# Optimization experiments

Measured on AMD Instinct MI355X. Metric: run time of the kernel, lower is better.

The kernel has to match this reference:

```python
import jax, jax.numpy as jnp
import numpy as np

V = 100000   # vertices
C = 64       # in channels
D = 64       # out channels
W = 8        # weight matrices
DEG = 16     # neighbors per vertex
E = V * DEG  # edges


def setup_inputs() -> dict:
    key = jax.random.key(0)
    k = jax.random.split(key, 6)
    data = jax.random.normal(k[0], (V, C), dtype=jnp.float32)
    # fixed-degree adjacency: vertex i has DEG neighbors (arbitrary dst)
    edge_src = jnp.repeat(jnp.arange(V, dtype=jnp.int32), DEG)        # [E] sorted
    edge_dst = jax.random.randint(k[1], (E,), 0, V, dtype=jnp.int32)  # [E]
    edge_vals = jnp.full((E,), 1.0 / DEG, dtype=jnp.float32)          # row-normalized
    var_u = 0.1 * jax.random.normal(k[2], (C, W), dtype=jnp.float32)
    var_c = 0.1 * jax.random.normal(k[3], (W,), dtype=jnp.float32)
    var_w = 0.1 * jax.random.normal(k[4], (W, C, D), dtype=jnp.float32)
    var_b = 0.1 * jax.random.normal(k[5], (D,), dtype=jnp.float32)
    return {"data": data, "edge_src": edge_src, "edge_dst": edge_dst,
            "edge_vals": edge_vals, "var_u": var_u, "var_c": var_c,
            "var_w": var_w, "var_b": var_b}


def reference(data, edge_src, edge_dst, edge_vals, var_u, var_c, var_w, var_b):
    # translation_invariant=True => var_v = -var_u
    num_v = data.shape[0]
    x_u = data @ var_u            # [V, W]
    x_v = data @ (-var_u)         # [V, W]
    # edge logits and exp-normalize over the W weight matrices (softmax == exp/sum)
    logits = x_u[edge_src] + x_v[edge_dst] + var_c   # [E, W]
    q = jax.nn.softmax(logits, axis=-1)              # [E, W]
    # gathered neighbor features, pre-scaled by adjacency values
    x_sep = data[edge_dst] * edge_vals[:, None]      # [E, C]
    y = jnp.zeros((num_v, var_w.shape[-1]), dtype=data.dtype)
    for m in range(var_c.shape[0]):  # small fixed loop over W weight matrices
        agg = jax.ops.segment_sum(q[:, m:m + 1] * x_sep, edge_src,
                                  num_segments=num_v)  # [V, C]
        y = y + agg @ var_w[m]                          # [V, D]
    return y + var_b
```

## Files before the change

### kernel.cpp

```cpp
#include <hip/hip_runtime.h>

typedef _Float16 half2_t __attribute__((ext_vector_type(2)));
typedef _Float16 half8_t __attribute__((ext_vector_type(8)));
typedef __attribute__((ext_vector_type(4))) float f32x4;

#define NV 100000
#define NTILE 6250
#define GRID 512
#define LDSZ 81920

#define VMWAIT(N) asm volatile("s_waitcnt vmcnt(" #N ")" ::: "memory")
#define LGKM0     asm volatile("s_waitcnt lgkmcnt(0)" ::: "memory")
#define FENCE     asm volatile("" ::: "memory")

__device__ __forceinline__ unsigned cvt_pk_u(float a, float b) {
  auto h = __builtin_amdgcn_cvt_pkrtz(a, b);
  return __builtin_bit_cast(unsigned, h);
}
__device__ __forceinline__ half2_t u2h(unsigned u) { return __builtin_bit_cast(half2_t, u); }
__device__ __forceinline__ unsigned h2u(half2_t h) { return __builtin_bit_cast(unsigned, h); }
__device__ __forceinline__ unsigned dup_lo(unsigned q) {
  return __builtin_amdgcn_perm(q, q, 0x01000100u);
}
__device__ __forceinline__ unsigned dup_hi(unsigned q) {
  return __builtin_amdgcn_perm(q, q, 0x03020302u);
}
__device__ __forceinline__ void load16_to_lds(const void* g, void* s) {
  __builtin_amdgcn_global_load_lds(
      (const __attribute__((address_space(1))) unsigned int*)g,
      (__attribute__((address_space(3))) unsigned int*)s, 16, 0, 0);
}

__global__ __launch_bounds__(256) void k0_prep_w(const float* __restrict__ var_w,
                                                 unsigned short* __restrict__ Bt) {
  int t = blockIdx.x * 256 + threadIdx.x;
  if (t >= 64 * 512) return;
  int d = t >> 9, k = t & 511;
  _Float16 h = (_Float16)var_w[k * 64 + d];
  Bt[t] = __builtin_bit_cast(unsigned short, h);
}

__global__ __launch_bounds__(256) void k1_prep(const float* __restrict__ data,
                                               const float* __restrict__ var_u,
                                               unsigned short* __restrict__ data_h,
                                               unsigned short* __restrict__ xu_h) {
  __shared__ float u_lds[512];
  int tid = threadIdx.x;
  u_lds[tid] = var_u[tid];
  u_lds[tid + 256] = var_u[tid + 256];
  __syncthreads();
  int v = blockIdx.x * 256 + tid;
  if (v >= NV) return;
  const float4* dp = (const float4*)(data + v * 64);
  float acc[8];
#pragma unroll
  for (int w = 0; w < 8; ++w) acc[w] = 0.f;
  uint4* ob = (uint4*)(data_h + v * 64);
#pragma unroll
  for (int q = 0; q < 8; ++q) {
    float4 a4 = dp[q * 2], b4 = dp[q * 2 + 1];
    int c0 = q * 8;
#pragma unroll
    for (int w = 0; w < 8; ++w)
      acc[w] += a4.x * u_lds[(c0 + 0) * 8 + w] + a4.y * u_lds[(c0 + 1) * 8 + w]
              + a4.z * u_lds[(c0 + 2) * 8 + w] + a4.w * u_lds[(c0 + 3) * 8 + w]
              + b4.x * u_lds[(c0 + 4) * 8 + w] + b4.y * u_lds[(c0 + 5) * 8 + w]
              + b4.z * u_lds[(c0 + 6) * 8 + w] + b4.w * u_lds[(c0 + 7) * 8 + w];
    uint4 pk;
    pk.x = cvt_pk_u(a4.x, a4.y); pk.y = cvt_pk_u(a4.z, a4.w);
    pk.z = cvt_pk_u(b4.x, b4.y); pk.w = cvt_pk_u(b4.z, b4.w);
    ob[q] = pk;
  }
  uint4 xp;
  xp.x = cvt_pk_u(acc[0], acc[1]); xp.y = cvt_pk_u(acc[2], acc[3]);
  xp.z = cvt_pk_u(acc[4], acc[5]); xp.w = cvt_pk_u(acc[6], acc[7]);
  *(uint4*)(xu_h + v * 8) = xp;
}

__global__ __launch_bounds__(256, 2) void k2_main(
    const unsigned short* __restrict__ data_h,
    const unsigned short* __restrict__ xu_h,
    const int* __restrict__ edge_dst,
    const float* __restrict__ edge_vals,
    const unsigned short* __restrict__ Bt,
    const float* __restrict__ var_c,
    const float* __restrict__ var_b,
    float* __restrict__ y) {
  extern __shared__ __align__(16) char smem[];
  char* XB0  = smem;
  char* XUD0 = smem + 65536;
  char* LIN0 = smem + 73728;

  int tid = threadIdx.x;
  int wave = tid >> 6;
  int l = tid & 63;
  int q4 = l >> 4;
  int row = l & 15;
  int col = row + wave * 16;
  int lsw = (l & 56) | ((l & 7) ^ q4);

  uint4 btf[16];
#pragma unroll
  for (int ks = 0; ks < 16; ++ks)
    btf[ks] = *(const uint4*)(Bt + (col * 512 + ks * 32 + q4 * 8));
  float c8[8];
#pragma unroll
  for (int m = 0; m < 8; ++m) c8[m] = var_c[m];
  float bias = var_b[col];

#define LIN_DMA(SL, TS)                                                        \
  { char* lb_ = LIN0 + (SL) * 2048;                                            \
    if ((wave & 1) == 0)                                                       \
      load16_to_lds(edge_dst + (size_t)(TS) * 256 + l * 4, lb_);               \
    else                                                                       \
      load16_to_lds(edge_vals + (size_t)(TS) * 256 + l * 4, lb_ + 1024); }
#define XUD_DMA(SL, LSL)                                                       \
  { const int* ld_ = (const int*)(LIN0 + (LSL) * 2048);                        \
    int dv_ = ld_[wave * 64 + lsw];                                            \
    load16_to_lds(xu_h + (size_t)dv_ * 8, XUD0 + (SL) * 4096 + wave * 1024); }
#define X_DMA(SL, LSL)                                                         \
  { const int* ld_ = (const int*)(LIN0 + (LSL) * 2048);                        \
    _Pragma("unroll")                                                          \
    for (int s_ = 0; s_ < 8; ++s_) {                                           \
      int r_ = wave * 64 + s_ * 8 + (l >> 3);                                  \
      int dv_ = ld_[r_];                                                       \
      load16_to_lds(data_h + (size_t)dv_ * 64 + (l & 7) * 8,                   \
                    XB0 + (SL) * 32768 + (wave * 64 + s_ * 8) * 128); } }

  int t0 = blockIdx.x;
  int tG1 = (t0 + GRID < NTILE) ? t0 + GRID : t0;
  int tG2 = (t0 + 2 * GRID < NTILE) ? t0 + 2 * GRID : t0;
  FENCE;
  LIN_DMA(0, t0);
  LIN_DMA(1, tG1);
  LIN_DMA(2, tG2);
  FENCE;
  uint4 xsA = *(const uint4*)(xu_h + ((size_t)t0 * 16 + wave * 4 + q4) * 8);
  uint4 xsB = *(const uint4*)(xu_h + ((size_t)tG1 * 16 + wave * 4 + q4) * 8);
  VMWAIT(0);
  __builtin_amdgcn_s_barrier();
  FENCE;
  XUD_DMA(0, 0);
  X_DMA(0, 0);
  FENCE;
  VMWAIT(0);
  __builtin_amdgcn_s_barrier();

  int kc = 0;
  for (int t = t0; t < NTILE; t += GRID, ++kc) {
    int slc = kc & 1, lslc = kc & 3;
    int sl1 = (kc + 1) & 1, lsl1 = (kc + 1) & 3, lsl3 = (kc + 3) & 3;
    int t2c = (t + 2 * GRID < NTILE) ? t + 2 * GRID : t;
    int t3c = (t + 3 * GRID < NTILE) ? t + 3 * GRID : t;
    const char* XBt = XB0 + slc * 32768;
    char* XUDt = XUD0 + slc * 4096;
    const char* LINt = LIN0 + lslc * 2048;

    FENCE;
    XUD_DMA(sl1, lsl1);
    X_DMA(sl1, lsl1);
    FENCE;

    {
      uint4 xd4 = *(const uint4*)(XUDt + (wave * 64 + l) * 16);
      float evv = ((const float*)(LINt + 1024))[wave * 64 + lsw];
      half2_t xm01 = u2h(xsA.x), xm23 = u2h(xsA.y), xm45 = u2h(xsA.z), xm67 = u2h(xsA.w);
      half2_t xd01 = u2h(xd4.x), xd23 = u2h(xd4.y), xd45 = u2h(xd4.z), xd67 = u2h(xd4.w);
      float ex0 = __expf((float)xm01[0] - (float)xd01[0] + c8[0]);
      float ex1 = __expf((float)xm01[1] - (float)xd01[1] + c8[1]);
      float ex2 = __expf((float)xm23[0] - (float)xd23[0] + c8[2]);
      float ex3 = __expf((float)xm23[1] - (float)xd23[1] + c8[3]);
      float ex4 = __expf((float)xm45[0] - (float)xd45[0] + c8[4]);
      float ex5 = __expf((float)xm45[1] - (float)xd45[1] + c8[5]);
      float ex6 = __expf((float)xm67[0] - (float)xd67[0] + c8[6]);
      float ex7 = __expf((float)xm67[1] - (float)xd67[1] + c8[7]);
      float ssum = ((ex0 + ex1) + (ex2 + ex3)) + ((ex4 + ex5) + (ex6 + ex7));
      float rs = __builtin_amdgcn_rcpf(ssum) * evv;
      uint4 qq;
      qq.x = cvt_pk_u(ex0 * rs, ex1 * rs);
      qq.y = cvt_pk_u(ex2 * rs, ex3 * rs);
      qq.z = cvt_pk_u(ex4 * rs, ex5 * rs);
      qq.w = cvt_pk_u(ex6 * rs, ex7 * rs);
      *(uint4*)(XUDt + (wave * 64 + l) * 16) = qq;
    }

    uint4 xsC = *(const uint4*)(xu_h + ((size_t)t2c * 16 + wave * 4 + q4) * 8);
    FENCE;
    LIN_DMA(lsl3, t3c);
    FENCE;

    {
      int v = q4, ck = row;
      half2_t acc2[16];
#pragma unroll
      for (int i = 0; i < 16; ++i) acc2[i] = half2_t{(_Float16)0, (_Float16)0};
#pragma unroll
      for (int j = 0; j < 16; ++j) {
        int qslot = v * 16 + (j & 8) + ((j & 7) ^ v);
        uint4 qv = *(const uint4*)(XUDt + (wave * 64 + qslot) * 16);
        uint2 xx = *(const uint2*)(XBt + (size_t)(wave * 64 + v * 16 + j) * 128 + ck * 8);
        half2_t xlo = u2h(xx.x), xhi = u2h(xx.y);
        unsigned qu;
        qu = qv.x;
        acc2[0]  += xlo * u2h(dup_lo(qu)); acc2[1]  += xhi * u2h(dup_lo(qu));
        acc2[2]  += xlo * u2h(dup_hi(qu)); acc2[3]  += xhi * u2h(dup_hi(qu));
        qu = qv.y;
        acc2[4]  += xlo * u2h(dup_lo(qu)); acc2[5]  += xhi * u2h(dup_lo(qu));
        acc2[6]  += xlo * u2h(dup_hi(qu)); acc2[7]  += xhi * u2h(dup_hi(qu));
        qu = qv.z;
        acc2[8]  += xlo * u2h(dup_lo(qu)); acc2[9]  += xhi * u2h(dup_lo(qu));
        acc2[10] += xlo * u2h(dup_hi(qu)); acc2[11] += xhi * u2h(dup_hi(qu));
        qu = qv.w;
        acc2[12] += xlo * u2h(dup_lo(qu)); acc2[13] += xhi * u2h(dup_lo(qu));
        acc2[14] += xlo * u2h(dup_hi(qu)); acc2[15] += xhi * u2h(dup_hi(qu));
      }
      int vg = wave * 4 + v;
      char* ab = (char*)XBt + vg * 2048;
#pragma unroll
      for (int m = 0; m < 8; ++m) {
        int bo = (m * 128 + ck * 8) ^ ((vg & 7) << 4);
        uint2 w2;
        w2.x = h2u(acc2[2 * m]);
        w2.y = h2u(acc2[2 * m + 1]);
        *(uint2*)(ab + bo) = w2;
      }
    }
    LGKM0;
    __builtin_amdgcn_s_barrier();

    {
      f32x4 C = {0.f, 0.f, 0.f, 0.f};
#pragma unroll
      for (int ks = 0; ks < 16; ++ks) {
        int bo = (ks * 64 + q4 * 16) ^ ((row & 7) << 4);
        half8_t af = *(const half8_t*)(XBt + row * 2048 + bo);
        C = __builtin_amdgcn_mfma_f32_16x16x32_f16(
            af, __builtin_bit_cast(half8_t, btf[ks]), C, 0, 0, 0);
      }
#pragma unroll
      for (int i = 0; i < 4; ++i)
        y[(size_t)(t * 16 + q4 * 4 + i) * 64 + col] = C[i] + bias;
    }
    LGKM0;
    VMWAIT(4);
    __builtin_amdgcn_s_barrier();

    xsA = xsB; xsB = xsC;
  }
  VMWAIT(0);
#undef LIN_DMA
#undef XUD_DMA
#undef X_DMA
}

extern "C" void kernel_launch(void* const* d_in, const int* in_sizes, int n_in,
                              void* d_out, int out_size, void* d_ws, size_t ws_size,
                              hipStream_t stream) {
  const float* data      = (const float*)d_in[0];
  const int*   edge_dst  = (const int*)d_in[2];
  const float* edge_vals = (const float*)d_in[3];
  const float* var_u     = (const float*)d_in[4];
  const float* var_c     = (const float*)d_in[5];
  const float* var_w     = (const float*)d_in[6];
  const float* var_b     = (const float*)d_in[7];
  float* y = (float*)d_out;

  char* ws = (char*)d_ws;
  unsigned short* data_h = (unsigned short*)ws;
  unsigned short* xu_h   = (unsigned short*)(ws + 12800000);
  unsigned short* Bt     = (unsigned short*)(ws + 14400000);

  hipFuncSetAttribute((const void*)k2_main,
                      hipFuncAttributeMaxDynamicSharedMemorySize, LDSZ);

  hipLaunchKernelGGL(k0_prep_w, dim3(128), dim3(256), 0, stream, var_w, Bt);
  hipLaunchKernelGGL(k1_prep, dim3((NV + 255) / 256), dim3(256), 0, stream,
                     data, var_u, data_h, xu_h);
  hipLaunchKernelGGL(k2_main, dim3(GRID), dim3(256), LDSZ, stream,
                     data_h, xu_h, edge_dst, edge_vals, Bt, var_c, var_b, y);
}
```

Measured before the change: 82.86 us.

## Compute per-vertex q-weighted aggregation with MFMA and transposed LDS reads

Replaces the packed-half2 VALU loop that forms the per-vertex 16-neighbor by 8-weight aggregation with 16x16x16 f16 MFMAs. It uses ds_read_b64_tr_b16 to read the gathered neighbor features transposed. The LDS layouts of the gathered rows, the q softmax weights and the aggregate tile are reorganized with new swizzles to suit the MFMA operands. Accumulation now happens in fp32 instead of fp16. Half of each MFMA output is discarded because only 8 weight columns are real, and the final aggregate write is restricted to rows below 8.

```diff
diff --git a/kernel.cpp b/kernel.cpp
--- a/kernel.cpp
+++ b/kernel.cpp
@@ -1,6 +1,7 @@
 #include <hip/hip_runtime.h>
 
 typedef _Float16 half2_t __attribute__((ext_vector_type(2)));
+typedef _Float16 half4_t __attribute__((ext_vector_type(4)));
 typedef _Float16 half8_t __attribute__((ext_vector_type(8)));
 typedef __attribute__((ext_vector_type(4))) float f32x4;
 
@@ -18,12 +19,8 @@
   return __builtin_bit_cast(unsigned, h);
 }
 __device__ __forceinline__ half2_t u2h(unsigned u) { return __builtin_bit_cast(half2_t, u); }
-__device__ __forceinline__ unsigned h2u(half2_t h) { return __builtin_bit_cast(unsigned, h); }
-__device__ __forceinline__ unsigned dup_lo(unsigned q) {
-  return __builtin_amdgcn_perm(q, q, 0x01000100u);
-}
-__device__ __forceinline__ unsigned dup_hi(unsigned q) {
-  return __builtin_amdgcn_perm(q, q, 0x03020302u);
+__device__ __forceinline__ unsigned lds_off(const void* p) {
+  return (unsigned)(size_t)(const __attribute__((address_space(3))) char*)p;
 }
 __device__ __forceinline__ void load16_to_lds(const void* g, void* s) {
   __builtin_amdgcn_global_load_lds(
@@ -97,7 +94,6 @@
   int q4 = l >> 4;
   int row = l & 15;
   int col = row + wave * 16;
-  int lsw = (l & 56) | ((l & 7) ^ q4);
 
   uint4 btf[16];
 #pragma unroll
@@ -116,16 +112,18 @@
       load16_to_lds(edge_vals + (size_t)(TS) * 256 + l * 4, lb_ + 1024); }
 #define XUD_DMA(SL, LSL)                                                       \
   { const int* ld_ = (const int*)(LIN0 + (LSL) * 2048);                        \
-    int dv_ = ld_[wave * 64 + lsw];                                            \
+    int dv_ = ld_[wave * 64 + l];                                              \
     load16_to_lds(xu_h + (size_t)dv_ * 8, XUD0 + (SL) * 4096 + wave * 1024); }
 #define X_DMA(SL, LSL)                                                         \
   { const int* ld_ = (const int*)(LIN0 + (LSL) * 2048);                        \
+    int j_ = ((l >> 3) & 3) * 4 + ((l >> 1) & 3);                              \
+    int ch0_ = ((l >> 5) << 1) | (l & 1);                                      \
     _Pragma("unroll")                                                          \
     for (int s_ = 0; s_ < 8; ++s_) {                                           \
-      int r_ = wave * 64 + s_ * 8 + (l >> 3);                                  \
-      int dv_ = ld_[r_];                                                       \
-      load16_to_lds(data_h + (size_t)dv_ * 64 + (l & 7) * 8,                   \
-                    XB0 + (SL) * 32768 + (wave * 64 + s_ * 8) * 128); } }
+      int dv_ = ld_[wave * 64 + (s_ >> 1) * 16 + j_];                          \
+      int ch_ = ch0_ + (s_ & 1) * 4;                                           \
+      load16_to_lds(data_h + (size_t)dv_ * 64 + ch_ * 8,                       \
+                    XB0 + (SL) * 32768 + wave * 8192 + s_ * 1024); } }
 
   int t0 = blockIdx.x;
   int tG1 = (t0 + GRID < NTILE) ? t0 + GRID : t0;
@@ -152,7 +150,7 @@
     int sl1 = (kc + 1) & 1, lsl1 = (kc + 1) & 3, lsl3 = (kc + 3) & 3;
     int t2c = (t + 2 * GRID < NTILE) ? t + 2 * GRID : t;
     int t3c = (t + 3 * GRID < NTILE) ? t + 3 * GRID : t;
-    const char* XBt = XB0 + slc * 32768;
+    char* XBt = XB0 + slc * 32768;
     char* XUDt = XUD0 + slc * 4096;
     const char* LINt = LIN0 + lslc * 2048;
 
@@ -163,7 +161,7 @@
 
     {
       uint4 xd4 = *(const uint4*)(XUDt + (wave * 64 + l) * 16);
-      float evv = ((const float*)(LINt + 1024))[wave * 64 + lsw];
+      float evv = ((const float*)(LINt + 1024))[wave * 64 + l];
       half2_t xm01 = u2h(xsA.x), xm23 = u2h(xsA.y), xm45 = u2h(xsA.z), xm67 = u2h(xsA.w);
       half2_t xd01 = u2h(xd4.x), xd23 = u2h(xd4.y), xd45 = u2h(xd4.z), xd67 = u2h(xd4.w);
       float ex0 = __expf((float)xm01[0] - (float)xd01[0] + c8[0]);
@@ -181,7 +179,14 @@
       qq.y = cvt_pk_u(ex2 * rs, ex3 * rs);
       qq.z = cvt_pk_u(ex4 * rs, ex5 * rs);
       qq.w = cvt_pk_u(ex6 * rs, ex7 * rs);
-      *(uint4*)(XUDt + (wave * 64 + l) * 16) = qq;
+      int vv = l >> 4, jq = (l >> 2) & 3, jl = l & 3;
+      char* qb = XUDt + wave * 1024 + vv * 256;
+#pragma unroll
+      for (int m = 0; m < 8; ++m) {
+        unsigned short hv = (unsigned short)((&qq.x)[m >> 1] >> ((m & 1) * 16));
+        int byte = (((m ^ vv) & 7) << 5) + (((jq ^ vv ^ m) & 3) << 3) + jl * 2;
+        *(unsigned short*)(qb + byte) = hv;
+      }
     }
 
     uint4 xsC = *(const uint4*)(xu_h + ((size_t)t2c * 16 + wave * 4 + q4) * 8);
@@ -190,39 +195,51 @@
     FENCE;
 
     {
-      int v = q4, ck = row;
-      half2_t acc2[16];
-#pragma unroll
-      for (int i = 0; i < 16; ++i) acc2[i] = half2_t{(_Float16)0, (_Float16)0};
-#pragma unroll
-      for (int j = 0; j < 16; ++j) {
-        int qslot = v * 16 + (j & 8) + ((j & 7) ^ v);
-        uint4 qv = *(const uint4*)(XUDt + (wave * 64 + qslot) * 16);
-        uint2 xx = *(const uint2*)(XBt + (size_t)(wave * 64 + v * 16 + j) * 128 + ck * 8);
-        half2_t xlo = u2h(xx.x), xhi = u2h(xx.y);
-        unsigned qu;
-        qu = qv.x;
-        acc2[0]  += xlo * u2h(dup_lo(qu)); acc2[1]  += xhi * u2h(dup_lo(qu));
-        acc2[2]  += xlo * u2h(dup_hi(qu)); acc2[3]  += xhi * u2h(dup_hi(qu));
-        qu = qv.y;
-        acc2[4]  += xlo * u2h(dup_lo(qu)); acc2[5]  += xhi * u2h(dup_lo(qu));
-        acc2[6]  += xlo * u2h(dup_hi(qu)); acc2[7]  += xhi * u2h(dup_hi(qu));
-        qu = qv.z;
-        acc2[8]  += xlo * u2h(dup_lo(qu)); acc2[9]  += xhi * u2h(dup_lo(qu));
-        acc2[10] += xlo * u2h(dup_hi(qu)); acc2[11] += xhi * u2h(dup_hi(qu));
-        qu = qv.w;
-        acc2[12] += xlo * u2h(dup_lo(qu)); acc2[13] += xhi * u2h(dup_lo(qu));
-        acc2[14] += xlo * u2h(dup_hi(qu)); acc2[15] += xhi * u2h(dup_hi(qu));
-      }
-      int vg = wave * 4 + v;
-      char* ab = (char*)XBt + vg * 2048;
-#pragma unroll
-      for (int m = 0; m < 8; ++m) {
-        int bo = (m * 128 + ck * 8) ^ ((vg & 7) << 4);
-        uint2 w2;
-        w2.x = h2u(acc2[2 * m]);
-        w2.y = h2u(acc2[2 * m + 1]);
-        *(uint2*)(ab + bo) = w2;
+      uint2 qfr[4];
+#pragma unroll
+      for (int vv = 0; vv < 4; ++vv) {
+        int srow = (row ^ vv) & 7;
+        int gsl = (q4 ^ vv ^ row) & 3;
+        qfr[vv] = *(const uint2*)(XUDt + wave * 1024 + vv * 256 + srow * 32 + gsl * 8);
+      }
+      unsigned xbase = lds_off(XBt + wave * 8192) + l * 8;
+      uint2 trd[16];
+#pragma unroll
+      for (int vv = 0; vv < 4; ++vv)
+#pragma unroll
+        for (int cb = 0; cb < 4; ++cb) {
+          unsigned a_ = xbase + vv * 2048 + cb * 512;
+          asm volatile("ds_read_b64_tr_b16 %0, %1"
+                       : "=v"(trd[vv * 4 + cb]) : "v"(a_) : "memory");
+        }
+      LGKM0;
+      __builtin_amdgcn_sched_barrier(0);
+      f32x4 D[16];
+#pragma unroll
+      for (int vv = 0; vv < 4; ++vv)
+#pragma unroll
+        for (int cb = 0; cb < 4; ++cb) {
+          f32x4 z = {0.f, 0.f, 0.f, 0.f};
+          D[vv * 4 + cb] = __builtin_amdgcn_mfma_f32_16x16x16f16(
+              __builtin_bit_cast(half4_t, trd[vv * 4 + cb]),
+              __builtin_bit_cast(half4_t, qfr[vv]), z, 0, 0, 0);
+        }
+      if (row < 8) {
+#pragma unroll
+        for (int vv = 0; vv < 4; ++vv) {
+          int vg = wave * 4 + vv;
+          char* ab = XBt + vg * 2048;
+#pragma unroll
+          for (int cb = 0; cb < 4; ++cb) {
+            f32x4 d4 = D[vv * 4 + cb];
+            uint2 w2;
+            w2.x = cvt_pk_u(d4[0], d4[1]);
+            w2.y = cvt_pk_u(d4[2], d4[3]);
+            int byte = (row * 128 + cb * 32 + q4 * 8) ^ ((vg & 7) << 4)
+                       ^ ((row & 3) << 5);
+            *(uint2*)(ab + byte) = w2;
+          }
+        }
       }
     }
     LGKM0;
@@ -232,7 +249,7 @@
       f32x4 C = {0.f, 0.f, 0.f, 0.f};
 #pragma unroll
       for (int ks = 0; ks < 16; ++ks) {
-        int bo = (ks * 64 + q4 * 16) ^ ((row & 7) << 4);
+        int bo = (ks * 64 + q4 * 16) ^ ((row & 7) << 4) ^ (((ks >> 1) & 3) << 5);
         half8_t af = *(const half8_t*)(XBt + row * 2048 + bo);
         C = __builtin_amdgcn_mfma_f32_16x16x32_f16(
             af, __builtin_bit_cast(half8_t, btf[ks]), C, 0, 0, 0);
```

Result: faster. 76.26 us (-8.0%).
